# Performance work log

Hardware: AMD Instinct MI355X
Metric: run time of the kernel (lower is better)

Reference implementation:

```python
import jax, jax.numpy as jnp
import numpy as np

N_NODES = 100000
N_EDGES = 3200000
N_GRAPHS = 64
IN_DIM = 128
HID = 64
NUM_FAMILIES = 64
CPF = 3  # centroids per family
GOODWARE_C = 5
BN_EPS = 1e-5


def setup_inputs() -> dict:
    key = jax.random.key(0)
    ks = jax.random.split(key, 16)
    x = jax.random.normal(ks[0], (N_NODES, IN_DIM), dtype=jnp.float32)
    edge_index = jax.random.randint(ks[1], (2, N_EDGES), 0, N_NODES, dtype=jnp.int32)
    batch = jnp.sort(jax.random.randint(ks[2], (N_NODES,), 0, N_GRAPHS, dtype=jnp.int32))
    def lin(k, fin, fout):
        s = 1.0 / np.sqrt(fin)
        return jax.random.uniform(k, (fin, fout), jnp.float32, -s, s)
    W1 = lin(ks[3], IN_DIM, HID); b1 = jnp.zeros((HID,), jnp.float32)
    W2 = lin(ks[4], HID, HID);    b2 = jnp.zeros((HID,), jnp.float32)
    W3 = lin(ks[5], HID, HID);    b3 = jnp.zeros((HID,), jnp.float32)
    g1 = jnp.ones((HID,), jnp.float32); be1 = jnp.zeros((HID,), jnp.float32)
    g2 = jnp.ones((HID,), jnp.float32); be2 = jnp.zeros((HID,), jnp.float32)
    g3 = jnp.ones((HID,), jnp.float32); be3 = jnp.zeros((HID,), jnp.float32)
    cm = jax.random.normal(ks[6], (NUM_FAMILIES * CPF, HID), jnp.float32) / np.sqrt(HID)
    cg = jax.random.normal(ks[7], (GOODWARE_C, HID), jnp.float32) / np.sqrt(HID)
    temp = jnp.ones((1,), jnp.float32)
    return dict(x=x, edge_index=edge_index, batch=batch,
                W1=W1, b1=b1, g1=g1, be1=be1,
                W2=W2, b2=b2, g2=g2, be2=be2,
                W3=W3, b3=b3, g3=g3, be3=be3,
                cg=cg, cm=cm, temp=temp)


def _gcn_conv(h_in, W, b, row, col, dinv_sqrt):
    # GCNConv: lin -> symmetric-normalized scatter-add (with self loops) -> bias
    h = h_in @ W  # [N, HID]
    enorm = (dinv_sqrt[row] * dinv_sqrt[col])[:, None]  # [E, 1]
    agg = jax.ops.segment_sum(h[row] * enorm, col, num_segments=N_NODES)
    agg = agg + h * (dinv_sqrt * dinv_sqrt)[:, None]  # self-loop term (norm = 1/deg)
    return agg + b


def _bn(x, gamma, beta):
    # training-mode BatchNorm1d over node dim (biased variance)
    m = jnp.mean(x, axis=0)
    v = jnp.mean((x - m) ** 2, axis=0)
    return (x - m) * jax.lax.rsqrt(v + BN_EPS) * gamma + beta


def reference(x, edge_index, batch,
              W1, b1, g1, be1, W2, b2, g2, be2, W3, b3, g3, be3,
              cg, cm, temp):
    row, col = edge_index[0], edge_index[1]
    # degree including self loop
    deg = jax.ops.segment_sum(jnp.ones((N_EDGES,), jnp.float32), col,
                              num_segments=N_NODES) + 1.0
    dinv_sqrt = jax.lax.rsqrt(deg)

    h = jax.nn.relu(_bn(_gcn_conv(x, W1, b1, row, col, dinv_sqrt), g1, be1))
    h = jax.nn.relu(_bn(_gcn_conv(h, W2, b2, row, col, dinv_sqrt), g2, be2))
    h = _bn(_gcn_conv(h, W3, b3, row, col, dinv_sqrt), g3, be3)

    # global mean pool over graphs
    sums = jax.ops.segment_sum(h, batch, num_segments=N_GRAPHS)
    cnts = jax.ops.segment_sum(jnp.ones((N_NODES,), jnp.float32), batch,
                               num_segments=N_GRAPHS)
    emb = sums / jnp.maximum(cnts, 1.0)[:, None]  # [B, HID]

    # centroid classifier (phase='family')
    gd = jnp.sum((emb[:, None, :] - cg[None, :, :]) ** 2, axis=2)  # [B, 5]
    md = jnp.sum((emb[:, None, :] - cm[None, :, :]) ** 2, axis=2)  # [B, F*CPF]
    md = md.reshape(N_GRAPHS, NUM_FAMILIES, CPF)
    min_g = jnp.min(gd, axis=1)          # [B]
    min_m = jnp.min(md, axis=2)          # [B, F]
    logits = jnp.concatenate([(-min_g / temp)[:, None], -min_m / temp], axis=1)
    return logits
```

## Files before the change

### kernel.cpp

```cpp
#include <hip/hip_runtime.h>
#include <math.h>

#define N_NODES 100000
#define N_EDGES 3200000
#define N_GRAPHS 64
#define IN_DIM 128
#define HID 64
#define BN_EPS 1e-5f

#define PSHIFT 9
#define PBS 512
#define NPB ((N_NODES + PBS - 1) / PBS)
#define PART_BLOCKS 256
#define CHUNK_E (N_EDGES / PART_BLOCKS)

#define QBOUND 25000
#define AGG_BLOCKS 2048

typedef unsigned short ushort_t;

__device__ __forceinline__ float bflo(unsigned u) { return __uint_as_float(u << 16); }
__device__ __forceinline__ float bfhi(unsigned u) { return __uint_as_float(u & 0xFFFF0000u); }
__device__ __forceinline__ float bfu(ushort_t u) { return __uint_as_float((unsigned)u << 16); }
__device__ __forceinline__ unsigned f2bf(float f) {
  unsigned u = __float_as_uint(f);
  return (u + 0x7FFFu + ((u >> 16) & 1u)) >> 16;
}


__global__ __launch_bounds__(256) void ghist_k(const int* __restrict__ ei,
                                               int* __restrict__ gh) {
  __shared__ int h[NPB];
  for (int i = threadIdx.x; i < NPB; i += 256) h[i] = 0;
  __syncthreads();
  const int4* d4 = (const int4*)(ei + N_EDGES);
  int n4 = N_EDGES / 4;
  int stride = gridDim.x * 256;
  for (int i = blockIdx.x * 256 + threadIdx.x; i < n4; i += stride) {
    int4 d = d4[i];
    atomicAdd(&h[d.x >> PSHIFT], 1);
    atomicAdd(&h[d.y >> PSHIFT], 1);
    atomicAdd(&h[d.z >> PSHIFT], 1);
    atomicAdd(&h[d.w >> PSHIFT], 1);
  }
  __syncthreads();
  for (int i = threadIdx.x; i < NPB; i += 256) {
    int v = h[i];
    if (v) atomicAdd(&gh[i], v);
  }
}

__global__ __launch_bounds__(256) void gscan_k(const int* __restrict__ gh,
                                               int* __restrict__ boff,
                                               int* __restrict__ gcur) {
  __shared__ int sa[256], sb[256];
  int t = threadIdx.x;
  int v = (t < NPB) ? gh[t] : 0;
  sa[t] = v;
  __syncthreads();
  int* src = sa; int* dst = sb;
  for (int o = 1; o < 256; o <<= 1) {
    dst[t] = src[t] + ((t >= o) ? src[t - o] : 0);
    __syncthreads();
    int* tmp = src; src = dst; dst = tmp;
  }
  if (t < NPB) {
    int excl = src[t] - v;
    boff[t] = excl;
    gcur[t] = excl;
    if (t == NPB - 1) boff[NPB] = src[t];
  }
}

__global__ __launch_bounds__(512) void part_k(const int* __restrict__ ei,
                                              int* __restrict__ gcur,
                                              unsigned* __restrict__ tmp) {
  __shared__ int lh[NPB];
  __shared__ int lcur[NPB];
  int t = threadIdx.x;
  for (int i = t; i < NPB; i += 512) lh[i] = 0;
  __syncthreads();
  int q0 = blockIdx.x * (CHUNK_E / 4);
  int q1 = q0 + CHUNK_E / 4;
  const int4* d4 = (const int4*)(ei + N_EDGES);
  const int4* s4 = (const int4*)ei;
  for (int i = q0 + t; i < q1; i += 512) {
    int4 d = d4[i];
    atomicAdd(&lh[d.x >> PSHIFT], 1);
    atomicAdd(&lh[d.y >> PSHIFT], 1);
    atomicAdd(&lh[d.z >> PSHIFT], 1);
    atomicAdd(&lh[d.w >> PSHIFT], 1);
  }
  __syncthreads();
  for (int i = t; i < NPB; i += 512) {
    int v = lh[i];
    lcur[i] = v ? atomicAdd(&gcur[i], v) : 0;
  }
  __syncthreads();
  for (int i = q0 + t; i < q1; i += 512) {
    int4 d = d4[i];
    int4 s = s4[i];
    int b0 = d.x >> PSHIFT, b1 = d.y >> PSHIFT, b2 = d.z >> PSHIFT, b3 = d.w >> PSHIFT;
    int p0 = atomicAdd(&lcur[b0], 1);
    int p1 = atomicAdd(&lcur[b1], 1);
    int p2 = atomicAdd(&lcur[b2], 1);
    int p3 = atomicAdd(&lcur[b3], 1);
    tmp[p0] = ((unsigned)(d.x & (PBS - 1)) << 17) | (unsigned)s.x;
    tmp[p1] = ((unsigned)(d.y & (PBS - 1)) << 17) | (unsigned)s.y;
    tmp[p2] = ((unsigned)(d.z & (PBS - 1)) << 17) | (unsigned)s.z;
    tmp[p3] = ((unsigned)(d.w & (PBS - 1)) << 17) | (unsigned)s.w;
  }
}

__global__ __launch_bounds__(512) void bwork_k(
    const unsigned* __restrict__ tmp, const int* __restrict__ boff,
    int* __restrict__ rp4, float* __restrict__ dinv, int* __restrict__ csr) {
  int b = blockIdx.x;
  int base = boff[b], end = boff[b + 1];
  int t = threadIdx.x;
  __shared__ int cnt[PBS * 4];
  __shared__ int cur[PBS * 4];
  __shared__ int sa[PBS], sb[PBS];
  for (int i = t; i < PBS * 4; i += 512) cnt[i] = 0;
  __syncthreads();
  int a0 = (base + 3) & ~3;
  int a1 = end & ~3;
  if (a1 < a0) { a0 = end; a1 = end; }
  const uint4* t4 = (const uint4*)tmp;
#define HIST1(U) { unsigned u_ = (U); int nl_ = u_ >> 17; int s_ = u_ & 0x1FFFF; \
    int qq_ = (s_ >= QBOUND) + (s_ >= 2*QBOUND) + (s_ >= 3*QBOUND); \
    atomicAdd(&cnt[nl_ * 4 + qq_], 1); }
  if (base + t < a0) HIST1(tmp[base + t]);
  for (int i = a0 / 4 + t; i < a1 / 4; i += 512) {
    uint4 u = t4[i];
    HIST1(u.x) HIST1(u.y) HIST1(u.z) HIST1(u.w)
  }
  if (a1 + t < end) HIST1(tmp[a1 + t]);
#undef HIST1
  __syncthreads();
  int c0 = cnt[t * 4], c1 = cnt[t * 4 + 1], c2 = cnt[t * 4 + 2], c3 = cnt[t * 4 + 3];
  int tsum = c0 + c1 + c2 + c3;
  sa[t] = tsum;
  __syncthreads();
  int* src_ = sa; int* dst_ = sb;
  for (int o = 1; o < PBS; o <<= 1) {
    dst_[t] = src_[t] + ((t >= o) ? src_[t - o] : 0);
    __syncthreads();
    int* z = src_; src_ = dst_; dst_ = z;
  }
  int nb = src_[t] - tsum;
  int o0 = nb, o1 = nb + c0, o2 = nb + c0 + c1, o3 = nb + c0 + c1 + c2;
  cur[t * 4] = o0; cur[t * 4 + 1] = o1; cur[t * 4 + 2] = o2; cur[t * 4 + 3] = o3;
  int n = b * PBS + t;
  if (n < N_NODES) {
    rp4[4 * n] = base + o0;
    rp4[4 * n + 1] = base + o1;
    rp4[4 * n + 2] = base + o2;
    rp4[4 * n + 3] = base + o3;
    dinv[n] = rsqrtf((float)(tsum + 1));
    if (n == N_NODES - 1) rp4[4 * N_NODES] = base + nb + tsum;
  }
  __syncthreads();
#define PLACE1(U) { unsigned u_ = (U); int nl_ = u_ >> 17; int s_ = u_ & 0x1FFFF; \
    int qq_ = (s_ >= QBOUND) + (s_ >= 2*QBOUND) + (s_ >= 3*QBOUND); \
    int p_ = atomicAdd(&cur[nl_ * 4 + qq_], 1); \
    csr[base + p_] = s_ << 7; }
  if (base + t < a0) PLACE1(tmp[base + t]);
  for (int i = a0 / 4 + t; i < a1 / 4; i += 512) {
    uint4 u = t4[i];
    PLACE1(u.x) PLACE1(u.y) PLACE1(u.z) PLACE1(u.w)
  }
  if (a1 + t < end) PLACE1(tmp[a1 + t]);
#undef PLACE1
}


template <int K, bool XBF16, bool APPLY, bool RELU>
__global__ __launch_bounds__(256) void gemm_k(
    const void* __restrict__ Xv, const float* __restrict__ W,
    const float* __restrict__ sums, const float* __restrict__ gamma,
    const float* __restrict__ beta,
    const float* __restrict__ dinv, ushort_t* __restrict__ out, int nrows) {
  constexpr int WROW = K + 1;
  __shared__ float wt[64 * WROW];
  __shared__ float xs[64 * 68];
  const int tid = threadIdx.x;
  const int tc = tid & 15;
  const int tr = tid >> 4;

  float sc4[4], sh4[4];
  if (APPLY) {
    const int kq = tid & 15;
#pragma unroll
    for (int t = 0; t < 4; ++t) {
      int kg = kq * 4 + t;
      float m = sums[kg] / (float)N_NODES;
      float v = sums[64 + kg] / (float)N_NODES - m * m;
      float s = gamma[kg] * rsqrtf(v + BN_EPS);
      sc4[t] = s;
      sh4[t] = beta[kg] - m * s;
    }
  }

  for (int idx = tid; idx < K * 64; idx += 256) {
    int k = idx >> 6, c = idx & 63;
    wt[c * WROW + k] = W[idx];
  }

  const int rowbase = blockIdx.x * 64;
  float acc[4][4] = {};

  for (int kc = 0; kc < K; kc += 64) {
    __syncthreads();
    {
      const int kq = tid & 15;
      const int rr = tid >> 4;
#pragma unroll
      for (int p = 0; p < 4; ++p) {
        int r = rr + p * 16;
        int grow = rowbase + r;
        float4 v = make_float4(0.f, 0.f, 0.f, 0.f);
        if (grow < nrows) {
          if (XBF16) {
            uint2 uv = *(const uint2*)((const char*)Xv + (size_t)grow * 128 + kq * 8);
            v = make_float4(bflo(uv.x), bfhi(uv.x), bflo(uv.y), bfhi(uv.y));
          } else {
            v = *(const float4*)((const float*)Xv + (size_t)grow * K + kc + kq * 4);
          }
        }
        if (APPLY) {
          v.x = v.x * sc4[0] + sh4[0];
          v.y = v.y * sc4[1] + sh4[1];
          v.z = v.z * sc4[2] + sh4[2];
          v.w = v.w * sc4[3] + sh4[3];
          if (RELU) {
            v.x = fmaxf(v.x, 0.f); v.y = fmaxf(v.y, 0.f);
            v.z = fmaxf(v.z, 0.f); v.w = fmaxf(v.w, 0.f);
          }
        }
        *(float4*)(xs + r * 68 + kq * 4) = v;
      }
    }
    __syncthreads();
#pragma unroll 4
    for (int k0 = 0; k0 < 64; k0 += 4) {
      float4 xv[4], wv[4];
#pragma unroll
      for (int i = 0; i < 4; ++i)
        xv[i] = *(const float4*)(xs + (tr * 4 + i) * 68 + k0);
#pragma unroll
      for (int j = 0; j < 4; ++j)
        wv[j] = *(const float4*)(wt + (4 * tc + j) * WROW + kc + k0);
#pragma unroll
      for (int i = 0; i < 4; ++i)
#pragma unroll
        for (int j = 0; j < 4; ++j)
          acc[i][j] += xv[i].x * wv[j].x + xv[i].y * wv[j].y +
                       xv[i].z * wv[j].z + xv[i].w * wv[j].w;
    }
  }

  char* ob = (char*)out;
#pragma unroll
  for (int i = 0; i < 4; ++i) {
    int grow = rowbase + tr * 4 + i;
    if (grow < nrows) {
      float dn = dinv[grow];
      uint2 o;
      o.x = f2bf(acc[i][0] * dn) | (f2bf(acc[i][1] * dn) << 16);
      o.y = f2bf(acc[i][2] * dn) | (f2bf(acc[i][3] * dn) << 16);
      *(uint2*)(ob + (size_t)grow * 128 + tc * 8) = o;
    }
  }
}


__global__ __launch_bounds__(256) void agg_k(
    const ushort_t* __restrict__ hs, const float* __restrict__ dinv,
    const int* __restrict__ rp4, const int* __restrict__ csr,
    const float* __restrict__ bias, ushort_t* __restrict__ out,
    float* __restrict__ sums) {
  const int tid = threadIdx.x;
  const int w = tid >> 6;
  const int lane = tid & 63;
  const int g = lane >> 4;
  const int q = lane & 15;
  const char* hb = (const char*)hs;
  char* ob = (char*)out;

  float4 bval = *(const float4*)(bias + q * 4);
  float4 s = make_float4(0.f, 0.f, 0.f, 0.f);
  float4 s2 = make_float4(0.f, 0.f, 0.f, 0.f);

  for (int n = blockIdx.x * 16 + w * 4 + g; n < N_NODES; n += AGG_BLOCKS * 16) {
    int r0 = rp4[4 * n];
    int cnt = rp4[4 * n + 4] - r0;
    float4 aA = {0, 0, 0, 0}, aB = {0, 0, 0, 0};
    int j = 0;
    for (; j + 8 <= cnt; j += 8) {
      int e0 = csr[r0 + j + 0], e1 = csr[r0 + j + 1];
      int e2 = csr[r0 + j + 2], e3 = csr[r0 + j + 3];
      int e4 = csr[r0 + j + 4], e5 = csr[r0 + j + 5];
      int e6 = csr[r0 + j + 6], e7 = csr[r0 + j + 7];
      uint2 v0 = *(const uint2*)(hb + (size_t)(unsigned)e0 + (q << 3));
      uint2 v1 = *(const uint2*)(hb + (size_t)(unsigned)e1 + (q << 3));
      uint2 v2 = *(const uint2*)(hb + (size_t)(unsigned)e2 + (q << 3));
      uint2 v3 = *(const uint2*)(hb + (size_t)(unsigned)e3 + (q << 3));
      uint2 v4 = *(const uint2*)(hb + (size_t)(unsigned)e4 + (q << 3));
      uint2 v5 = *(const uint2*)(hb + (size_t)(unsigned)e5 + (q << 3));
      uint2 v6 = *(const uint2*)(hb + (size_t)(unsigned)e6 + (q << 3));
      uint2 v7 = *(const uint2*)(hb + (size_t)(unsigned)e7 + (q << 3));
      aA.x += bflo(v0.x); aA.y += bfhi(v0.x); aA.z += bflo(v0.y); aA.w += bfhi(v0.y);
      aB.x += bflo(v1.x); aB.y += bfhi(v1.x); aB.z += bflo(v1.y); aB.w += bfhi(v1.y);
      aA.x += bflo(v2.x); aA.y += bfhi(v2.x); aA.z += bflo(v2.y); aA.w += bfhi(v2.y);
      aB.x += bflo(v3.x); aB.y += bfhi(v3.x); aB.z += bflo(v3.y); aB.w += bfhi(v3.y);
      aA.x += bflo(v4.x); aA.y += bfhi(v4.x); aA.z += bflo(v4.y); aA.w += bfhi(v4.y);
      aB.x += bflo(v5.x); aB.y += bfhi(v5.x); aB.z += bflo(v5.y); aB.w += bfhi(v5.y);
      aA.x += bflo(v6.x); aA.y += bfhi(v6.x); aA.z += bflo(v6.y); aA.w += bfhi(v6.y);
      aB.x += bflo(v7.x); aB.y += bfhi(v7.x); aB.z += bflo(v7.y); aB.w += bfhi(v7.y);
    }
    for (; j + 2 <= cnt; j += 2) {
      int e0 = csr[r0 + j + 0], e1 = csr[r0 + j + 1];
      uint2 v0 = *(const uint2*)(hb + (size_t)(unsigned)e0 + (q << 3));
      uint2 v1 = *(const uint2*)(hb + (size_t)(unsigned)e1 + (q << 3));
      aA.x += bflo(v0.x); aA.y += bfhi(v0.x); aA.z += bflo(v0.y); aA.w += bfhi(v0.y);
      aB.x += bflo(v1.x); aB.y += bfhi(v1.x); aB.z += bflo(v1.y); aB.w += bfhi(v1.y);
    }
    if (j < cnt) {
      int e0 = csr[r0 + j];
      uint2 v0 = *(const uint2*)(hb + (size_t)(unsigned)e0 + (q << 3));
      aA.x += bflo(v0.x); aA.y += bfhi(v0.x); aA.z += bflo(v0.y); aA.w += bfhi(v0.y);
    }
    uint2 u = *(const uint2*)(hb + ((size_t)n << 7) + (q << 3));
    float4 a;
    a.x = aA.x + aB.x + bflo(u.x);
    a.y = aA.y + aB.y + bfhi(u.x);
    a.z = aA.z + aB.z + bflo(u.y);
    a.w = aA.w + aB.w + bfhi(u.y);
    float dn = dinv[n];
    a.x = a.x * dn + bval.x; a.y = a.y * dn + bval.y;
    a.z = a.z * dn + bval.z; a.w = a.w * dn + bval.w;
    uint2 o;
    o.x = f2bf(a.x) | (f2bf(a.y) << 16);
    o.y = f2bf(a.z) | (f2bf(a.w) << 16);
    *(uint2*)(ob + ((size_t)n << 7) + (q << 3)) = o;
    s.x += a.x; s.y += a.y; s.z += a.z; s.w += a.w;
    s2.x += a.x * a.x; s2.y += a.y * a.y;
    s2.z += a.z * a.z; s2.w += a.w * a.w;
  }

  __shared__ float rs[16][64];
  __shared__ float rs2[16][64];
  *(float4*)(&rs[w * 4 + g][q * 4]) = s;
  *(float4*)(&rs2[w * 4 + g][q * 4]) = s2;
  __syncthreads();
  int c = tid & 63;
  int r0_ = tid >> 6;
  float a = rs[r0_][c] + rs[r0_ + 4][c] + rs[r0_ + 8][c] + rs[r0_ + 12][c];
  float a2 = rs2[r0_][c] + rs2[r0_ + 4][c] + rs2[r0_ + 8][c] + rs2[r0_ + 12][c];
  __syncthreads();
  rs[r0_][c] = a;
  rs2[r0_][c] = a2;
  __syncthreads();
  if (r0_ == 0) {
    atomicAdd(&sums[c], rs[0][c] + rs[1][c] + rs[2][c] + rs[3][c]);
    atomicAdd(&sums[64 + c], rs2[0][c] + rs2[1][c] + rs2[2][c] + rs2[3][c]);
  }
}


#define POOL_CHUNK 32
__global__ __launch_bounds__(256) void pool_k(
    const ushort_t* __restrict__ h, const float* __restrict__ sums,
    const float* __restrict__ gamma, const float* __restrict__ beta,
    const int* __restrict__ batch,
    float* __restrict__ psum, float* __restrict__ pcnt) {
  int w = threadIdx.x >> 6;
  int lane = threadIdx.x & 63;
  int start = (blockIdx.x * 4 + w) * POOL_CHUNK;
  if (start >= N_NODES) return;
  int end = min(start + POOL_CHUNK, N_NODES);
  float m = sums[lane] / (float)N_NODES;
  float v = sums[64 + lane] / (float)N_NODES - m * m;
  float sc = gamma[lane] * rsqrtf(v + BN_EPS);
  float sh = beta[lane] - m * sc;
  float acc = 0.f, cnt = 0.f;
  int cur = batch[start];
  for (int n = start; n < end; ++n) {
    int g = batch[n];
    if (g != cur) {
      atomicAdd(&psum[cur * 64 + lane], acc);
      if (lane == 0) atomicAdd(&pcnt[cur], cnt);
      acc = 0.f; cnt = 0.f; cur = g;
    }
    acc += bfu(h[(size_t)n * 64 + lane]) * sc + sh;
    cnt += 1.f;
  }
  atomicAdd(&psum[cur * 64 + lane], acc);
  if (lane == 0) atomicAdd(&pcnt[cur], cnt);
}


__global__ void classify_k(const float* __restrict__ psum, const float* __restrict__ pcnt,
                           const float* __restrict__ cg_, const float* __restrict__ cm,
                           const float* __restrict__ temp, float* __restrict__ out) {
  int g = blockIdx.x;
  int t = threadIdx.x;
  __shared__ float emb[64];
  __shared__ float dist[208];
  if (t < 64) emb[t] = psum[g * 64 + t] / fmaxf(pcnt[g], 1.0f);
  __syncthreads();
  if (t < 197) {
    const float* C = (t < 5) ? (cg_ + t * 64) : (cm + (t - 5) * 64);
    float d = 0.f;
#pragma unroll 8
    for (int k = 0; k < 64; ++k) {
      float df = emb[k] - C[k];
      d += df * df;
    }
    dist[t] = d;
  }
  __syncthreads();
  float tv = temp[0];
  if (t == 64) {
    float m = dist[0];
    for (int j = 1; j < 5; ++j) m = fminf(m, dist[j]);
    out[g * 65] = -m / tv;
  }
  if (t < 64) {
    float m = fminf(dist[5 + t * 3], fminf(dist[5 + t * 3 + 1], dist[5 + t * 3 + 2]));
    out[g * 65 + 1 + t] = -m / tv;
  }
}


extern "C" void kernel_launch(void* const* d_in, const int* in_sizes, int n_in,
                              void* d_out, int out_size, void* d_ws, size_t ws_size,
                              hipStream_t stream) {
  const float* x   = (const float*)d_in[0];
  const int* ei    = (const int*)d_in[1];
  const int* batch = (const int*)d_in[2];
  const float* W1 = (const float*)d_in[3];  const float* b1 = (const float*)d_in[4];
  const float* g1 = (const float*)d_in[5];  const float* be1 = (const float*)d_in[6];
  const float* W2 = (const float*)d_in[7];  const float* b2 = (const float*)d_in[8];
  const float* g2 = (const float*)d_in[9];  const float* be2 = (const float*)d_in[10];
  const float* W3 = (const float*)d_in[11]; const float* b3 = (const float*)d_in[12];
  const float* g3 = (const float*)d_in[13]; const float* be3 = (const float*)d_in[14];
  const float* cg_ = (const float*)d_in[15];
  const float* cm = (const float*)d_in[16];
  const float* temp = (const float*)d_in[17];
  float* out = (float*)d_out;

  char* ws = (char*)d_ws;
  size_t off = 0;
  auto alloc = [&](size_t bytes) -> void* {
    void* p = ws + off;
    off = (off + bytes + 255) & ~(size_t)255;
    return p;
  };
  int* gh        = (int*)alloc((size_t)NPB * 4);
  int* boff      = (int*)alloc((size_t)(NPB + 1) * 4);
  int* gcur      = (int*)alloc((size_t)NPB * 4);
  unsigned* tmp  = (unsigned*)alloc((size_t)N_EDGES * 4);
  int* csr       = (int*)alloc((size_t)N_EDGES * 4);
  int* rp4       = (int*)alloc((size_t)(4 * N_NODES + 1) * 4);
  float* dinv    = (float*)alloc((size_t)N_NODES * 4);
  ushort_t* hA   = (ushort_t*)alloc((size_t)N_NODES * 64 * 2);
  ushort_t* hB   = (ushort_t*)alloc((size_t)N_NODES * 64 * 2);
  float* sumsAll = (float*)alloc(3 * 128 * 4);
  float* psum    = (float*)alloc(64 * 64 * 4);
  float* pcnt    = (float*)alloc(64 * 4);

  hipMemsetAsync(gh, 0, (size_t)NPB * 4, stream);
  hipMemsetAsync(sumsAll, 0, 3 * 128 * 4, stream);
  hipMemsetAsync(psum, 0, 64 * 64 * 4, stream);
  hipMemsetAsync(pcnt, 0, 64 * 4, stream);

  const int NB_GEMM = (N_NODES + 63) / 64;
  const int NB_POOL = (N_NODES + POOL_CHUNK * 4 - 1) / (POOL_CHUNK * 4);

  ghist_k<<<512, 256, 0, stream>>>(ei, gh);
  gscan_k<<<1, 256, 0, stream>>>(gh, boff, gcur);
  part_k<<<PART_BLOCKS, 512, 0, stream>>>(ei, gcur, tmp);
  bwork_k<<<NPB, 512, 0, stream>>>(tmp, boff, rp4, dinv, csr);

  gemm_k<IN_DIM, false, false, false><<<NB_GEMM, 256, 0, stream>>>(x, W1, nullptr, nullptr, nullptr, dinv, hA, N_NODES);
  agg_k<<<AGG_BLOCKS, 256, 0, stream>>>(hA, dinv, rp4, csr, b1, hB, sumsAll);

  gemm_k<HID, true, true, true><<<NB_GEMM, 256, 0, stream>>>(hB, W2, sumsAll, g1, be1, dinv, hA, N_NODES);
  agg_k<<<AGG_BLOCKS, 256, 0, stream>>>(hA, dinv, rp4, csr, b2, hB, sumsAll + 128);

  gemm_k<HID, true, true, true><<<NB_GEMM, 256, 0, stream>>>(hB, W3, sumsAll + 128, g2, be2, dinv, hA, N_NODES);
  agg_k<<<AGG_BLOCKS, 256, 0, stream>>>(hA, dinv, rp4, csr, b3, hB, sumsAll + 256);

  pool_k<<<NB_POOL, 256, 0, stream>>>(hB, sumsAll + 256, g3, be3, batch, psum, pcnt);
  classify_k<<<N_GRAPHS, 256, 0, stream>>>(psum, pcnt, cg_, cm, temp, out);
}
```

Baseline: 589.1 us.

## Rewrite dense transform GEMM with bf16 MFMA 16x16x32 instructions

Replaces the FP32 shared-memory register-tiled GEMM with bf16 MFMA intrinsics. Each wave computes 16 rows by 64 columns, loading the activations straight from global memory into registers and the weights from LDS as bf16. The result is transposed through an LDS buffer so each row can be written with wide stores. The aim is to cut the ALU cost of the node-feature transform. In exchange, the fp32 input and the weights are now rounded to bf16, which lowers precision.

```diff
diff --git a/kernel.cpp b/kernel.cpp
--- a/kernel.cpp
+++ b/kernel.cpp
@@ -18,6 +18,8 @@
 #define AGG_BLOCKS 2048
 
 typedef unsigned short ushort_t;
+typedef __attribute__((ext_vector_type(8))) short bf16x8;
+typedef __attribute__((ext_vector_type(4))) float f32x4;
 
 __device__ __forceinline__ float bflo(unsigned u) { return __uint_as_float(u << 16); }
 __device__ __forceinline__ float bfhi(unsigned u) { return __uint_as_float(u & 0xFFFF0000u); }
@@ -179,97 +181,110 @@
 __global__ __launch_bounds__(256) void gemm_k(
     const void* __restrict__ Xv, const float* __restrict__ W,
     const float* __restrict__ sums, const float* __restrict__ gamma,
-    const float* __restrict__ beta,
-    const float* __restrict__ dinv, ushort_t* __restrict__ out, int nrows) {
-  constexpr int WROW = K + 1;
-  __shared__ float wt[64 * WROW];
-  __shared__ float xs[64 * 68];
+    const float* __restrict__ beta, const float* __restrict__ dinv,
+    ushort_t* __restrict__ out, int nrows) {
+  __shared__ ushort_t wt[64 * K];
+  __shared__ float scs[128], shs[128];
+  __shared__ float redo[64 * 65];
   const int tid = threadIdx.x;
-  const int tc = tid & 15;
-  const int tr = tid >> 4;
-
-  float sc4[4], sh4[4];
-  if (APPLY) {
-    const int kq = tid & 15;
-#pragma unroll
-    for (int t = 0; t < 4; ++t) {
-      int kg = kq * 4 + t;
-      float m = sums[kg] / (float)N_NODES;
-      float v = sums[64 + kg] / (float)N_NODES - m * m;
-      float s = gamma[kg] * rsqrtf(v + BN_EPS);
-      sc4[t] = s;
-      sh4[t] = beta[kg] - m * s;
-    }
-  }
+  const int wv = tid >> 6;
+  const int lane = tid & 63;
+  const int lm = lane & 15;
+  const int lq = lane >> 4;
 
   for (int idx = tid; idx < K * 64; idx += 256) {
     int k = idx >> 6, c = idx & 63;
-    wt[c * WROW + k] = W[idx];
-  }
+    wt[c * K + k] = (ushort_t)f2bf(W[idx]);
+  }
+  if (APPLY) {
+    for (int k = tid; k < K; k += 256) {
+      float m = sums[k] / (float)N_NODES;
+      float v = sums[64 + k] / (float)N_NODES - m * m;
+      float s = gamma[k] * rsqrtf(v + BN_EPS);
+      scs[k] = s;
+      shs[k] = beta[k] - m * s;
+    }
+  }
+  __syncthreads();
 
   const int rowbase = blockIdx.x * 64;
-  float acc[4][4] = {};
-
-  for (int kc = 0; kc < K; kc += 64) {
-    __syncthreads();
-    {
-      const int kq = tid & 15;
-      const int rr = tid >> 4;
+  const int grow = rowbase + wv * 16 + lm;
+  const bool valid = grow < nrows;
+  f32x4 acc0 = {0.f, 0.f, 0.f, 0.f};
+  f32x4 acc1 = acc0, acc2 = acc0, acc3 = acc0;
+
 #pragma unroll
-      for (int p = 0; p < 4; ++p) {
-        int r = rr + p * 16;
-        int grow = rowbase + r;
-        float4 v = make_float4(0.f, 0.f, 0.f, 0.f);
-        if (grow < nrows) {
-          if (XBF16) {
-            uint2 uv = *(const uint2*)((const char*)Xv + (size_t)grow * 128 + kq * 8);
-            v = make_float4(bflo(uv.x), bfhi(uv.x), bflo(uv.y), bfhi(uv.y));
-          } else {
-            v = *(const float4*)((const float*)Xv + (size_t)grow * K + kc + kq * 4);
+  for (int k0 = 0; k0 < K; k0 += 32) {
+    int kbase = k0 + lq * 8;
+    bf16x8 a = {0, 0, 0, 0, 0, 0, 0, 0};
+    if (valid) {
+      if (XBF16) {
+        uint4 u = *(const uint4*)((const char*)Xv + ((size_t)grow * 64 + kbase) * 2);
+        if (APPLY) {
+          float4 sc0 = *(const float4*)&scs[kbase];
+          float4 sc1 = *(const float4*)&scs[kbase + 4];
+          float4 sh0 = *(const float4*)&shs[kbase];
+          float4 sh1 = *(const float4*)&shs[kbase + 4];
+          float f0 = bflo(u.x) * sc0.x + sh0.x, f1 = bfhi(u.x) * sc0.y + sh0.y;
+          float f2 = bflo(u.y) * sc0.z + sh0.z, f3 = bfhi(u.y) * sc0.w + sh0.w;
+          float f4 = bflo(u.z) * sc1.x + sh1.x, f5 = bfhi(u.z) * sc1.y + sh1.y;
+          float f6 = bflo(u.w) * sc1.z + sh1.z, f7 = bfhi(u.w) * sc1.w + sh1.w;
+          if (RELU) {
+            f0 = fmaxf(f0, 0.f); f1 = fmaxf(f1, 0.f);
+            f2 = fmaxf(f2, 0.f); f3 = fmaxf(f3, 0.f);
+            f4 = fmaxf(f4, 0.f); f5 = fmaxf(f5, 0.f);
+            f6 = fmaxf(f6, 0.f); f7 = fmaxf(f7, 0.f);
           }
+          a[0] = (short)f2bf(f0); a[1] = (short)f2bf(f1);
+          a[2] = (short)f2bf(f2); a[3] = (short)f2bf(f3);
+          a[4] = (short)f2bf(f4); a[5] = (short)f2bf(f5);
+          a[6] = (short)f2bf(f6); a[7] = (short)f2bf(f7);
+        } else {
+          a = *(const bf16x8*)&u;
         }
-        if (APPLY) {
-          v.x = v.x * sc4[0] + sh4[0];
-          v.y = v.y * sc4[1] + sh4[1];
-          v.z = v.z * sc4[2] + sh4[2];
-          v.w = v.w * sc4[3] + sh4[3];
-          if (RELU) {
-            v.x = fmaxf(v.x, 0.f); v.y = fmaxf(v.y, 0.f);
-            v.z = fmaxf(v.z, 0.f); v.w = fmaxf(v.w, 0.f);
-          }
-        }
-        *(float4*)(xs + r * 68 + kq * 4) = v;
+      } else {
+        const float* xp = (const float*)Xv + (size_t)grow * K + kbase;
+        float4 xa = *(const float4*)xp;
+        float4 xb = *(const float4*)(xp + 4);
+        a[0] = (short)f2bf(xa.x); a[1] = (short)f2bf(xa.y);
+        a[2] = (short)f2bf(xa.z); a[3] = (short)f2bf(xa.w);
+        a[4] = (short)f2bf(xb.x); a[5] = (short)f2bf(xb.y);
+        a[6] = (short)f2bf(xb.z); a[7] = (short)f2bf(xb.w);
       }
     }
-    __syncthreads();
-#pragma unroll 4
-    for (int k0 = 0; k0 < 64; k0 += 4) {
-      float4 xv[4], wv[4];
+    bf16x8 b0 = *(const bf16x8*)(wt + (0 + lm) * K + kbase);
+    bf16x8 b1 = *(const bf16x8*)(wt + (16 + lm) * K + kbase);
+    bf16x8 b2 = *(const bf16x8*)(wt + (32 + lm) * K + kbase);
+    bf16x8 b3 = *(const bf16x8*)(wt + (48 + lm) * K + kbase);
+    acc0 = __builtin_amdgcn_mfma_f32_16x16x32_bf16(a, b0, acc0, 0, 0, 0);
+    acc1 = __builtin_amdgcn_mfma_f32_16x16x32_bf16(a, b1, acc1, 0, 0, 0);
+    acc2 = __builtin_amdgcn_mfma_f32_16x16x32_bf16(a, b2, acc2, 0, 0, 0);
+    acc3 = __builtin_amdgcn_mfma_f32_16x16x32_bf16(a, b3, acc3, 0, 0, 0);
+  }
+
 #pragma unroll
-      for (int i = 0; i < 4; ++i)
-        xv[i] = *(const float4*)(xs + (tr * 4 + i) * 68 + k0);
+  for (int r = 0; r < 4; ++r) {
+    int rr = wv * 16 + lq * 4 + r;
+    redo[rr * 65 + lm] = acc0[r];
+    redo[rr * 65 + 16 + lm] = acc1[r];
+    redo[rr * 65 + 32 + lm] = acc2[r];
+    redo[rr * 65 + 48 + lm] = acc3[r];
+  }
+  __syncthreads();
+  {
+    int r = tid >> 2;
+    int cq = (tid & 3) * 16;
+    int gr = rowbase + r;
+    if (gr < nrows) {
+      float dn = dinv[gr];
+      const float* sp = &redo[r * 65 + cq];
+      unsigned p[8];
 #pragma unroll
-      for (int j = 0; j < 4; ++j)
-        wv[j] = *(const float4*)(wt + (4 * tc + j) * WROW + kc + k0);
-#pragma unroll
-      for (int i = 0; i < 4; ++i)
-#pragma unroll
-        for (int j = 0; j < 4; ++j)
-          acc[i][j] += xv[i].x * wv[j].x + xv[i].y * wv[j].y +
-                       xv[i].z * wv[j].z + xv[i].w * wv[j].w;
-    }
-  }
-
-  char* ob = (char*)out;
-#pragma unroll
-  for (int i = 0; i < 4; ++i) {
-    int grow = rowbase + tr * 4 + i;
-    if (grow < nrows) {
-      float dn = dinv[grow];
-      uint2 o;
-      o.x = f2bf(acc[i][0] * dn) | (f2bf(acc[i][1] * dn) << 16);
-      o.y = f2bf(acc[i][2] * dn) | (f2bf(acc[i][3] * dn) << 16);
-      *(uint2*)(ob + (size_t)grow * 128 + tc * 8) = o;
+      for (int i = 0; i < 8; ++i)
+        p[i] = f2bf(sp[2 * i] * dn) | (f2bf(sp[2 * i + 1] * dn) << 16);
+      char* ob = (char*)out + ((size_t)gr * 64 + cq) * 2;
+      *(uint4*)ob = make_uint4(p[0], p[1], p[2], p[3]);
+      *(uint4*)(ob + 16) = make_uint4(p[4], p[5], p[6], p[7]);
     }
   }
 }
```

Result: faster. 565.7 us (-4.0%).
